# Kernel optimization log

Hardware: AMD Instinct MI355X
Metric: run time of the kernel (lower is better)

## Reference

```python
import jax, jax.numpy as jnp
import numpy as np

EPS = 1e-5

def _layernorm(x, g, b):
    mu = jnp.mean(x, axis=-1, keepdims=True)
    var = jnp.var(x, axis=-1, keepdims=True)
    return (x - mu) * jax.lax.rsqrt(var + EPS) * g + b

def setup_inputs() -> dict:
    key = jax.random.key(0)
    ks = jax.random.split(key, 12)
    E, N, H, OUT = 640000, 40000, 128, 1
    s = 1.0 / np.sqrt(H)
    s2 = 1.0 / np.sqrt(2 * H)
    return {
        "y": jax.random.normal(ks[0], (E, H), dtype=jnp.float32),
        "src": jax.random.randint(ks[1], (E,), 0, N),
        "dst": jax.random.randint(ks[2], (E,), 0, N),
        "n_nodes": N,
        "ln_g": jnp.ones((H,), jnp.float32),
        "ln_b": jnp.zeros((H,), jnp.float32),
        "Wl": jax.random.uniform(ks[3], (H, H), jnp.float32, -s, s),
        "bl": jax.random.uniform(ks[4], (H,), jnp.float32, -s, s),
        "Wr": jax.random.uniform(ks[5], (H, H), jnp.float32, -s, s),
        "br": jax.random.uniform(ks[6], (H,), jnp.float32, -s, s),
        "ln2_g": jnp.ones((2 * H,), jnp.float32),
        "ln2_b": jnp.zeros((2 * H,), jnp.float32),
        "W1": jax.random.uniform(ks[7], (2 * H, H), jnp.float32, -s2, s2),
        "b1": jax.random.uniform(ks[8], (H,), jnp.float32, -s2, s2),
        "W2": jax.random.uniform(ks[9], (H, OUT), jnp.float32, -s, s),
        "b2": jax.random.uniform(ks[10], (OUT,), jnp.float32, -s, s),
    }

def reference(y, src, dst, n_nodes, ln_g, ln_b, Wl, bl, Wr, br, ln2_g, ln2_b, W1, b1, W2, b2):
    # Gate each edge: LayerNorm -> Linear -> Sigmoid (left and right gates)
    yn = _layernorm(y, ln_g, ln_b)                       # [E, H]
    l_gate = jax.nn.sigmoid(yn @ Wl + bl)                # [E, H]
    r_gate = jax.nn.sigmoid(yn @ Wr + br)                # [E, H]
    # copy_e + mean reduce onto destination nodes (mean over incoming edges)
    cnt = jax.ops.segment_sum(jnp.ones((dst.shape[0],), y.dtype), dst, num_segments=n_nodes)
    denom = jnp.maximum(cnt, 1.0)[:, None]               # avoid div-by-zero; isolated nodes stay 0
    aleft = jax.ops.segment_sum(l_gate, dst, num_segments=n_nodes) / denom   # [N, H]
    aright = jax.ops.segment_sum(r_gate, dst, num_segments=n_nodes) / denom  # [N, H]
    # Per-edge MLP on concatenated src/dst node aggregates
    h = jnp.concatenate([aleft[src], aright[dst]], axis=1)  # [E, 2H]
    h = _layernorm(h, ln2_g, ln2_b)
    h = jax.nn.elu(h @ W1 + b1)                           # dropout is identity at inference
    return h @ W2 + b2                                    # [E, n_out]
```

## Files before the change

kernel.cpp:

```cpp
#include <hip/hip_runtime.h>
#include <hip/hip_bf16.h>

#define LN_EPS 1e-5f

typedef __attribute__((ext_vector_type(8))) short bf16x8;
typedef __attribute__((ext_vector_type(4))) float f32x4;

__device__ __forceinline__ float sigmoid_fast(float x) {
    return __builtin_amdgcn_rcpf(1.0f + __expf(-x));
}
__device__ __forceinline__ ushort f2bf(float x) {
    __hip_bfloat16 h = __float2bfloat16(x);
    return __builtin_bit_cast(ushort, h);
}
__device__ __forceinline__ int xcd_swz(int bid, int nwg) {
    const int q = nwg >> 3, r = nwg & 7;
    const int xcd = bid & 7, idx = bid >> 3;
    return (xcd < r ? xcd * (q + 1) : r * (q + 1) + (xcd - r) * q) + idx;
}
__device__ __forceinline__ int gperm(int l) {
    return (l & ~63) | (((l >> 2) & 3) << 4) | (((l >> 4) & 3) << 2) | (l & 3);
}
__device__ __forceinline__ void gload_lds16(const void* g, void* l) {
    __builtin_amdgcn_global_load_lds((const __attribute__((address_space(1))) void*)g,
                                     (__attribute__((address_space(3))) void*)l, 16, 0, 0);
}

struct WsPtrs {
    float *aggL, *aggR, *rd;
    int *ideg, *ioff, *icur, *elist, *epos;
    ushort *WgF, *W1F;
    float *gwb, *nstL, *nstR;
    int N;
};
__device__ __forceinline__ WsPtrs ws_ptrs(float* ws, const int* n_nodes_p, int E) {
    WsPtrs p;
    p.N    = *n_nodes_p;
    p.aggL = ws;
    p.aggR = ws + (size_t)p.N * 128;
    p.rd   = ws + (size_t)p.N * 256;
    p.ideg = (int*)(ws + (size_t)p.N * 257);
    p.ioff = p.ideg + p.N;
    p.icur = p.ioff + p.N + 1;
    p.elist = p.icur + p.N;
    p.epos  = p.elist + E;
    p.WgF = (ushort*)(((uintptr_t)(p.epos + E) + 15) & ~(uintptr_t)15);
    p.W1F = p.WgF + 32768;
    p.gwb = (float*)(p.W1F + 32768);
    p.nstL = p.gwb + 384;
    p.nstR = p.nstL + 2 * p.N;
    return p;
}

__global__ void init_kernel(float* __restrict__ ws, const int* __restrict__ n_nodes_p, int E) {
    WsPtrs p = ws_ptrs(ws, n_nodes_p, E);
    const long long stride = (long long)gridDim.x * blockDim.x;
    const long long tid = (long long)blockIdx.x * blockDim.x + threadIdx.x;
    const long long nf = (long long)p.N * 256;
    for (long long i = tid; i < nf; i += stride) ws[i] = 0.0f;
    for (long long i = tid; i < p.N; i += stride) p.ideg[i] = 0;
}

__global__ void hist_kernel(const int* __restrict__ dst, float* __restrict__ ws,
                            const int* __restrict__ n_nodes_p, int E) {
    WsPtrs p = ws_ptrs(ws, n_nodes_p, E);
    const int i = blockIdx.x * blockDim.x + threadIdx.x;
    if (i < E) atomicAdd(&p.ideg[dst[i]], 1);
}

__global__ __launch_bounds__(256) void scan_kernel(float* __restrict__ ws,
                                                   const int* __restrict__ n_nodes_p, int E) {
    WsPtrs p = ws_ptrs(ws, n_nodes_p, E);
    __shared__ int wsum[4];
    __shared__ int carry_s;
    const int t = threadIdx.x;
    const int lane = t & 63, wid = t >> 6;
    if (t == 0) carry_s = 0;
    __syncthreads();
    for (int base = 0; base < p.N; base += 1024) {
        const int i0 = base + t * 4;
        const int v0 = (i0 + 0 < p.N) ? p.ideg[i0 + 0] : 0;
        const int v1 = (i0 + 1 < p.N) ? p.ideg[i0 + 1] : 0;
        const int v2 = (i0 + 2 < p.N) ? p.ideg[i0 + 2] : 0;
        const int v3 = (i0 + 3 < p.N) ? p.ideg[i0 + 3] : 0;
        const int s = v0 + v1 + v2 + v3;
        int sc = s;
        #pragma unroll
        for (int off = 1; off < 64; off <<= 1) {
            const int n = __shfl_up(sc, off);
            if (lane >= off) sc += n;
        }
        if (lane == 63) wsum[wid] = sc;
        __syncthreads();
        int woff = 0;
        #pragma unroll
        for (int w = 0; w < 4; ++w) if (w < wid) woff += wsum[w];
        const int carry = carry_s;
        __syncthreads();
        const int excl = carry + woff + (sc - s);
        if (i0 + 0 < p.N) { p.ioff[i0+0] = excl;          p.icur[i0+0] = excl;          p.rd[i0+0] = 1.0f / fmaxf((float)v0, 1.0f); }
        if (i0 + 1 < p.N) { p.ioff[i0+1] = excl+v0;       p.icur[i0+1] = excl+v0;       p.rd[i0+1] = 1.0f / fmaxf((float)v1, 1.0f); }
        if (i0 + 2 < p.N) { p.ioff[i0+2] = excl+v0+v1;    p.icur[i0+2] = excl+v0+v1;    p.rd[i0+2] = 1.0f / fmaxf((float)v2, 1.0f); }
        if (i0 + 3 < p.N) { p.ioff[i0+3] = excl+v0+v1+v2; p.icur[i0+3] = excl+v0+v1+v2; p.rd[i0+3] = 1.0f / fmaxf((float)v3, 1.0f); }
        if (t == 255) carry_s = carry + woff + sc;
        __syncthreads();
    }
    if (t == 0) p.ioff[p.N] = carry_s;
}

__global__ void scatter_kernel(const int* __restrict__ dst, float* __restrict__ ws,
                               const int* __restrict__ n_nodes_p, int E) {
    WsPtrs p = ws_ptrs(ws, n_nodes_p, E);
    const int i = blockIdx.x * blockDim.x + threadIdx.x;
    if (i < E) {
        const int pos = atomicAdd(&p.icur[dst[i]], 1);
        p.elist[pos] = i;
        p.epos[i] = (pos & ~63) | gperm(pos & 63);
    }
}

__global__ void prep_w_kernel(const float* __restrict__ Wl, const float* __restrict__ Wr,
                              const float* __restrict__ W1,
                              const float* __restrict__ ln2_g, const float* __restrict__ ln2_b,
                              const float* __restrict__ b1,
                              float* __restrict__ ws, const int* __restrict__ n_nodes_p, int E) {
    WsPtrs p = ws_ptrs(ws, n_nodes_p, E);
    const int i = blockIdx.x * blockDim.x + threadIdx.x;
    if (i < 32768) {
        const int i8 = i & 7, lane = (i >> 3) & 63, kf = (i >> 9) & 3, nblk = i >> 11;
        const int k = kf * 32 + (lane >> 4) * 8 + i8;
        const int n = nblk * 16 + (lane & 15);
        const float val = (n < 128) ? Wl[k * 128 + n] : Wr[k * 128 + (n - 128)];
        p.WgF[i] = f2bf(val);
    } else if (i < 65536) {
        const int j = i - 32768;
        const int i8 = j & 7, lane = (j >> 3) & 63, kf = (j >> 9) & 7, nblk = j >> 12;
        const int k = kf * 32 + (lane >> 4) * 8 + i8;
        const int n = nblk * 16 + (lane & 15);
        p.W1F[j] = f2bf(W1[k * 128 + n]);
    } else if (i < 65664) {
        const int j = i - 65536;
        float gsL = 0.f, gsR = 0.f, bs = 0.f;
        for (int k = 0; k < 128; ++k) {
            const float wt = W1[k * 128 + j];
            const float wb = W1[(k + 128) * 128 + j];
            gsL += ln2_g[k] * wt;
            gsR += ln2_g[k + 128] * wb;
            bs  += ln2_b[k] * wt + ln2_b[k + 128] * wb;
        }
        p.gwb[j]       = gsL;
        p.gwb[128 + j] = gsR;
        p.gwb[256 + j] = bs + b1[j];
    }
}

__global__ __launch_bounds__(256) void ln_y_kernel(
    const float* __restrict__ y,
    const float* __restrict__ ln_g, const float* __restrict__ ln_b,
    float* __restrict__ ws, const int* __restrict__ n_nodes_p, int E,
    ushort* __restrict__ ynb)
{
    WsPtrs p = ws_ptrs(ws, n_nodes_p, E);
    const int t = threadIdx.x;
    const int e = blockIdx.x * 64 + (t >> 2);
    const int sub = t & 3;
    if (e >= E) return;

    const float* yr = y + (size_t)e * 128;
    float v[32];
    float s = 0.f, sq = 0.f;
    #pragma unroll
    for (int i = 0; i < 8; ++i) {
        const float4 q = *reinterpret_cast<const float4*>(yr + sub * 32 + i * 4);
        v[i*4+0] = q.x; v[i*4+1] = q.y; v[i*4+2] = q.z; v[i*4+3] = q.w;
        s  += q.x + q.y + q.z + q.w;
        sq += q.x*q.x + q.y*q.y + q.z*q.z + q.w*q.w;
    }
    s  += __shfl_xor(s, 1);  s  += __shfl_xor(s, 2);
    sq += __shfl_xor(sq, 1); sq += __shfl_xor(sq, 2);
    const float mu = s * (1.f / 128.f);
    const float rstd = rsqrtf(sq * (1.f / 128.f) - mu * mu + LN_EPS);

    ushort* dstrow = ynb + (size_t)p.epos[e] * 128 + sub * 32;
    #pragma unroll
    for (int i = 0; i < 4; ++i) {
        uint w32[4];
        #pragma unroll
        for (int h2 = 0; h2 < 4; ++h2) {
            const int c = sub * 32 + i * 8 + h2 * 2;
            const float x0 = (v[i*8 + h2*2 + 0] - mu) * rstd * ln_g[c + 0] + ln_b[c + 0];
            const float x1 = (v[i*8 + h2*2 + 1] - mu) * rstd * ln_g[c + 1] + ln_b[c + 1];
            w32[h2] = (uint)f2bf(x0) | ((uint)f2bf(x1) << 16);
        }
        *reinterpret_cast<uint4*>(dstrow + i * 8) = make_uint4(w32[0], w32[1], w32[2], w32[3]);
    }
}

__global__ __launch_bounds__(512) void gates_kernel(
    const float* __restrict__ y, const int* __restrict__ dst,
    const float* __restrict__ ln_g, const float* __restrict__ ln_b,
    const float* __restrict__ bl, const float* __restrict__ br,
    float* __restrict__ ws, const int* __restrict__ n_nodes_p, int E,
    const ushort* __restrict__ ynb)
{
    __shared__ ushort sA[128 * 128];
    __shared__ int sNode[128];

    WsPtrs p = ws_ptrs(ws, n_nodes_p, E);
    char* sAb = reinterpret_cast<char*>(sA);
    const int t = threadIdx.x;
    const int bid = xcd_swz(blockIdx.x, gridDim.x);
    const int s0 = bid * 128;
    const int lane = t & 63;
    const int w8 = t >> 6;

    if (t < 128) {
        const int j = s0 + t;
        const int eid = (j < E) ? p.elist[j] : -1;
        sNode[t] = (eid >= 0) ? dst[eid] : -1;
    }

    if (ynb) {
        const char* ybase = (const char*)ynb + (size_t)s0 * 256;
        #pragma unroll
        for (int i = 0; i < 4; ++i) {
            const int chunk = w8 + i * 8;
            const int L = chunk * 1024 + lane * 16;
            const int b = L ^ (((L >> 8) & 7) << 4);
            gload_lds16(ybase + b, sAb + chunk * 1024);
        }
    } else {
        const int r = t >> 2, sub = t & 3;
        const int je = s0 + gperm(r);
        const int eid = (je < E) ? p.elist[je] : 0;
        const float* yr = y + (size_t)eid * 128;
        float v[32];
        float s = 0.f, sq = 0.f;
        #pragma unroll
        for (int i = 0; i < 8; ++i) {
            const float4 q = *reinterpret_cast<const float4*>(yr + sub * 32 + i * 4);
            v[i*4+0] = q.x; v[i*4+1] = q.y; v[i*4+2] = q.z; v[i*4+3] = q.w;
            s  += q.x + q.y + q.z + q.w;
            sq += q.x*q.x + q.y*q.y + q.z*q.z + q.w*q.w;
        }
        s  += __shfl_xor(s, 1);  s  += __shfl_xor(s, 2);
        sq += __shfl_xor(sq, 1); sq += __shfl_xor(sq, 2);
        const float mu = s * (1.f / 128.f);
        const float rstd = rsqrtf(sq * (1.f / 128.f) - mu * mu + LN_EPS);
        #pragma unroll
        for (int i = 0; i < 4; ++i) {
            uint w32[4];
            #pragma unroll
            for (int h2 = 0; h2 < 4; ++h2) {
                const int c = sub * 32 + i * 8 + h2 * 2;
                const float x0 = (v[i*8 + h2*2 + 0] - mu) * rstd * ln_g[c + 0] + ln_b[c + 0];
                const float x1 = (v[i*8 + h2*2 + 1] - mu) * rstd * ln_g[c + 1] + ln_b[c + 1];
                w32[h2] = (uint)f2bf(x0) | ((uint)f2bf(x1) << 16);
            }
            int byte = r * 256 + sub * 64 + i * 16;
            byte ^= ((byte >> 8) & 7) << 4;
            *reinterpret_cast<uint4*>(sAb + byte) = make_uint4(w32[0], w32[1], w32[2], w32[3]);
        }
    }
    __syncthreads();

    const int rowh = w8 >> 2, colw = w8 & 3;
    const int lhi = lane >> 4, llo = lane & 15;

    f32x4 acc[4][4];
    #pragma unroll
    for (int m = 0; m < 4; ++m)
        #pragma unroll
        for (int n = 0; n < 4; ++n) acc[m][n] = (f32x4){0.f, 0.f, 0.f, 0.f};

    #pragma unroll
    for (int kf = 0; kf < 4; ++kf) {
        bf16x8 a[4], b[4];
        #pragma unroll
        for (int m = 0; m < 4; ++m) {
            const int row = rowh * 64 + m * 16 + llo;
            int byte = row * 256 + kf * 64 + lhi * 16;
            byte ^= ((byte >> 8) & 7) << 4;
            a[m] = *reinterpret_cast<const bf16x8*>(sAb + byte);
        }
        #pragma unroll
        for (int nf = 0; nf < 4; ++nf) {
            const int nblk = colw * 4 + nf;
            b[nf] = *reinterpret_cast<const bf16x8*>(p.WgF + ((size_t)(nblk * 4 + kf) * 64 + lane) * 8);
        }
        #pragma unroll
        for (int m = 0; m < 4; ++m)
            #pragma unroll
            for (int nf = 0; nf < 4; ++nf)
                acc[m][nf] = __builtin_amdgcn_mfma_f32_16x16x32_bf16(a[m], b[nf], acc[m][nf], 0, 0, 0);
    }

    const int g = colw >> 1;
    float* ag = g ? p.aggR : p.aggL;
    const float* bp = g ? br : bl;
    const int lcol0 = (colw & 1) * 64 + llo;
    float bias[4];
    #pragma unroll
    for (int nf = 0; nf < 4; ++nf) bias[nf] = bp[lcol0 + nf * 16];

    float run0 = 0.f, run1 = 0.f, run2 = 0.f, run3 = 0.f;
    int rnode = -1;
    #pragma unroll
    for (int m = 0; m < 4; ++m) {
        #pragma unroll
        for (int j = 0; j < 4; ++j) {
            const int el = rowh * 64 + lhi * 16 + m * 4 + j;
            const int node = sNode[el];
            const float v0 = sigmoid_fast(acc[m][0][j] + bias[0]);
            const float v1 = sigmoid_fast(acc[m][1][j] + bias[1]);
            const float v2 = sigmoid_fast(acc[m][2][j] + bias[2]);
            const float v3 = sigmoid_fast(acc[m][3][j] + bias[3]);
            if (node != rnode) {
                if (rnode >= 0) {
                    float* dest = ag + (size_t)rnode * 128 + lcol0;
                    atomicAdd(dest +  0, run0);
                    atomicAdd(dest + 16, run1);
                    atomicAdd(dest + 32, run2);
                    atomicAdd(dest + 48, run3);
                }
                rnode = node;
                run0 = v0; run1 = v1; run2 = v2; run3 = v3;
            } else {
                run0 += v0; run1 += v1; run2 += v2; run3 += v3;
            }
        }
    }
    if (rnode >= 0) {
        float* dest = ag + (size_t)rnode * 128 + lcol0;
        atomicAdd(dest +  0, run0);
        atomicAdd(dest + 16, run1);
        atomicAdd(dest + 32, run2);
        atomicAdd(dest + 48, run3);
    }
}

__global__ __launch_bounds__(512) void node_mlp_kernel(
    const float* __restrict__ ln2_g,
    float* __restrict__ ws, const int* __restrict__ n_nodes_p, int E)
{
    __shared__ ushort sA[128 * 256];

    WsPtrs p = ws_ptrs(ws, n_nodes_p, E);
    char* sAb = reinterpret_cast<char*>(sA);
    const int t = threadIdx.x;
    const int n0 = blockIdx.x * 128;

    {
        const int r = t >> 2, sub = t & 3;
        const int n = n0 + r;
        const bool vld = n < p.N;
        const int nn = vld ? n : (p.N - 1);
        const float* base = ((sub < 2) ? p.aggL : p.aggR) + (size_t)nn * 128 + (sub & 1) * 64;
        const float scale = vld ? p.rd[nn] : 0.f;
        const int cb = ((sub >> 1) << 7) + ((sub & 1) << 6);

        float s = 0.f, sq = 0.f;
        #pragma unroll
        for (int ii = 0; ii < 8; ++ii) {
            const float4 qa = *reinterpret_cast<const float4*>(base + ii * 8);
            const float4 qb = *reinterpret_cast<const float4*>(base + ii * 8 + 4);
            s  += qa.x + qa.y + qa.z + qa.w + qb.x + qb.y + qb.z + qb.w;
            sq += qa.x*qa.x + qa.y*qa.y + qa.z*qa.z + qa.w*qa.w
                + qb.x*qb.x + qb.y*qb.y + qb.z*qb.z + qb.w*qb.w;
        }
        s *= scale; sq *= scale * scale;
        s  += __shfl_xor(s, 1);
        sq += __shfl_xor(sq, 1);
        if (vld && sub == 0) { p.nstL[2*n] = s; p.nstL[2*n+1] = sq; }
        if (vld && sub == 2) { p.nstR[2*n] = s; p.nstR[2*n+1] = sq; }
        const float mu_n = s * (1.f / 128.f);

        #pragma unroll
        for (int ii = 0; ii < 8; ++ii) {
            const float4 qa = *reinterpret_cast<const float4*>(base + ii * 8);
            const float4 qb = *reinterpret_cast<const float4*>(base + ii * 8 + 4);
            const float xs[8] = { qa.x*scale - mu_n, qa.y*scale - mu_n, qa.z*scale - mu_n, qa.w*scale - mu_n,
                                  qb.x*scale - mu_n, qb.y*scale - mu_n, qb.z*scale - mu_n, qb.w*scale - mu_n };
            uint w32[4];
            #pragma unroll
            for (int h2 = 0; h2 < 4; ++h2) {
                const int c = cb + ii * 8 + h2 * 2;
                w32[h2] = (uint)f2bf(xs[h2*2+0] * ln2_g[c+0]) |
                          ((uint)f2bf(xs[h2*2+1] * ln2_g[c+1]) << 16);
            }
            int byte = r * 512 + cb * 2 + ii * 16;
            byte ^= ((byte >> 9) & 7) << 4;
            *reinterpret_cast<uint4*>(sAb + byte) = make_uint4(w32[0], w32[1], w32[2], w32[3]);
        }
    }
    __syncthreads();

    const int lane = t & 63;
    const int w8 = t >> 6;
    const int rowh = w8 >> 2, colw = w8 & 3;
    const int half = colw >> 1;
    const int lhi = lane >> 4, llo = lane & 15;

    f32x4 acc[4][4];
    #pragma unroll
    for (int m = 0; m < 4; ++m)
        #pragma unroll
        for (int n = 0; n < 4; ++n) acc[m][n] = (f32x4){0.f, 0.f, 0.f, 0.f};

    #pragma unroll
    for (int kfl = 0; kfl < 4; ++kfl) {
        bf16x8 a[4], b[4];
        #pragma unroll
        for (int m = 0; m < 4; ++m) {
            const int row = rowh * 64 + m * 16 + llo;
            int byte = row * 512 + half * 256 + kfl * 64 + lhi * 16;
            byte ^= ((byte >> 9) & 7) << 4;
            a[m] = *reinterpret_cast<const bf16x8*>(sAb + byte);
        }
        #pragma unroll
        for (int nf = 0; nf < 4; ++nf) {
            const int nblk = (colw & 1) * 4 + nf;
            const int kf = half * 4 + kfl;
            b[nf] = *reinterpret_cast<const bf16x8*>(p.W1F + ((size_t)(nblk * 8 + kf) * 64 + lane) * 8);
        }
        #pragma unroll
        for (int m = 0; m < 4; ++m)
            #pragma unroll
            for (int nf = 0; nf < 4; ++nf)
                acc[m][nf] = __builtin_amdgcn_mfma_f32_16x16x32_bf16(a[m], b[nf], acc[m][nf], 0, 0, 0);
    }

    ushort* u16 = (ushort*)(half ? p.aggR : p.aggL);
    #pragma unroll
    for (int m = 0; m < 4; ++m) {
        #pragma unroll
        for (int j = 0; j < 4; ++j) {
            const int n = n0 + rowh * 64 + m * 16 + lhi * 4 + j;
            if (n < p.N) {
                const int col = (colw & 1) * 64 + llo;
                #pragma unroll
                for (int nf = 0; nf < 4; ++nf)
                    u16[(size_t)n * 256 + col + nf * 16] = f2bf(acc[m][nf][j]);
            }
        }
    }
}

__global__ __launch_bounds__(256) void edge_out_kernel(
    const int* __restrict__ src, const int* __restrict__ dst,
    const float* __restrict__ W2, const float* __restrict__ b2,
    float* __restrict__ ws, const int* __restrict__ n_nodes_p,
    float* __restrict__ out, int E)
{
    WsPtrs p = ws_ptrs(ws, n_nodes_p, E);
    const ushort* uLb = (const ushort*)p.aggL;
    const ushort* uRb = (const ushort*)p.aggR;
    const int t = threadIdx.x;
    const int lane = t & 63;
    const int wv = blockIdx.x * 4 + (t >> 6);
    const int nw = gridDim.x * 4;
    const int span = (E + nw - 1) / nw;
    const int j0 = wv * span;
    const int j1 = min(E, j0 + span);

    const float2 gwl = *reinterpret_cast<const float2*>(p.gwb + lane * 2);
    const float2 gwr = *reinterpret_cast<const float2*>(p.gwb + 128 + lane * 2);
    const float2 bw  = *reinterpret_cast<const float2*>(p.gwb + 256 + lane * 2);
    const float2 w2  = *reinterpret_cast<const float2*>(W2 + lane * 2);
    const float b2v = b2[0];

    auto body = [&](int j, float& accv, int& eidv) {
        const int eid = p.elist[j];
        const int s = src[eid], d = dst[eid];
        const uint ulp = *reinterpret_cast<const uint*>(uLb + (size_t)s * 256 + lane * 2);
        const uint urp = *reinterpret_cast<const uint*>(uRb + (size_t)d * 256 + lane * 2);
        const float ulx = __builtin_bit_cast(float, ulp << 16);
        const float uly = __builtin_bit_cast(float, ulp & 0xffff0000u);
        const float urx = __builtin_bit_cast(float, urp << 16);
        const float ury = __builtin_bit_cast(float, urp & 0xffff0000u);
        const float2 nsl = *reinterpret_cast<const float2*>(p.nstL + 2 * s);
        const float2 nsr = *reinterpret_cast<const float2*>(p.nstR + 2 * d);
        const float mu = (nsl.x + nsr.x) * (1.f / 256.f);
        const float var = (nsl.y + nsr.y) * (1.f / 256.f) - mu * mu;
        const float rstd = rsqrtf(var + LN_EPS);
        const float dL = nsl.x * (1.f / 128.f) - mu;
        const float dR = nsr.x * (1.f / 128.f) - mu;
        float x0 = rstd * (ulx + urx + dL * gwl.x + dR * gwr.x) + bw.x;
        float x1 = rstd * (uly + ury + dL * gwl.y + dR * gwr.y) + bw.y;
        x0 = x0 > 0.f ? x0 : __expf(x0) - 1.f;
        x1 = x1 > 0.f ? x1 : __expf(x1) - 1.f;
        accv = x0 * w2.x + x1 * w2.y;
        eidv = eid;
    };

    int j = j0;
    for (; j + 1 < j1; j += 2) {
        float a0, a1; int e0, e1;
        body(j, a0, e0);
        body(j + 1, a1, e1);
        #pragma unroll
        for (int m = 32; m >= 1; m >>= 1) {
            a0 += __shfl_xor(a0, m);
            a1 += __shfl_xor(a1, m);
        }
        if (lane == 0) { out[e0] = a0 + b2v; out[e1] = a1 + b2v; }
    }
    if (j < j1) {
        float a0; int e0;
        body(j, a0, e0);
        #pragma unroll
        for (int m = 32; m >= 1; m >>= 1) a0 += __shfl_xor(a0, m);
        if (lane == 0) out[e0] = a0 + b2v;
    }
}

extern "C" void kernel_launch(void* const* d_in, const int* in_sizes, int n_in,
                              void* d_out, int out_size, void* d_ws, size_t ws_size,
                              hipStream_t stream) {
    const float* y       = (const float*)d_in[0];
    const int*   src     = (const int*)d_in[1];
    const int*   dst     = (const int*)d_in[2];
    const int*   n_nodes = (const int*)d_in[3];
    const float* ln_g    = (const float*)d_in[4];
    const float* ln_b    = (const float*)d_in[5];
    const float* Wl      = (const float*)d_in[6];
    const float* bl      = (const float*)d_in[7];
    const float* Wr      = (const float*)d_in[8];
    const float* br      = (const float*)d_in[9];
    const float* ln2_g   = (const float*)d_in[10];
    const float* ln2_b   = (const float*)d_in[11];
    const float* W1      = (const float*)d_in[12];
    const float* b1      = (const float*)d_in[13];
    const float* W2      = (const float*)d_in[14];
    const float* b2      = (const float*)d_in[15];
    float* out = (float*)d_out;
    float* ws  = (float*)d_ws;

    const int E = in_sizes[0] / 128;
    const int eb = (E + 127) / 128;
    const int N_MAX = 40000;

    const size_t need = (size_t)(E + 128) * 256;
    const bool use_pre = ws_size >= need + (96ull << 20);
    ushort* ynb = use_pre
        ? (ushort*)(((uintptr_t)ws + ws_size - need) & ~(uintptr_t)255)
        : nullptr;

    init_kernel<<<2048, 256, 0, stream>>>(ws, n_nodes, E);
    hist_kernel<<<(E + 255) / 256, 256, 0, stream>>>(dst, ws, n_nodes, E);
    scan_kernel<<<1, 256, 0, stream>>>(ws, n_nodes, E);
    scatter_kernel<<<(E + 255) / 256, 256, 0, stream>>>(dst, ws, n_nodes, E);
    prep_w_kernel<<<257, 256, 0, stream>>>(Wl, Wr, W1, ln2_g, ln2_b, b1, ws, n_nodes, E);
    if (use_pre)
        ln_y_kernel<<<(E + 63) / 64, 256, 0, stream>>>(y, ln_g, ln_b, ws, n_nodes, E, ynb);
    gates_kernel<<<eb, 512, 0, stream>>>(y, dst, ln_g, ln_b, bl, br, ws, n_nodes, E, ynb);
    node_mlp_kernel<<<(N_MAX + 127) / 128, 512, 0, stream>>>(ln2_g, ws, n_nodes, E);
    edge_out_kernel<<<2048, 256, 0, stream>>>(src, dst, W2, b2, ws, n_nodes, out, E);
}
```

Measured before the change: 560.0 us.

## Shrink gates tile to 64 edges per block and cache dst row in edge_out

The gates kernel now handles 64 sorted edges per 512-thread block instead of 128. Each wave covers all 64 rows and 32 output columns, which halves LDS and accumulator registers and adds a launch_bounds occupancy hint, at the cost of more blocks and reloading weight fragments per block. Separately, edge_out reuses the destination node's aggregate row and stats when consecutive edges share a dst, saving redundant gathers since edges are sorted by dst. Smaller tiles may flush more atomics at segment boundaries.

```diff
diff --git a/kernel.cpp b/kernel.cpp
--- a/kernel.cpp
+++ b/kernel.cpp
@@ -196,25 +196,25 @@
     }
 }
 
-__global__ __launch_bounds__(512) void gates_kernel(
+__global__ __launch_bounds__(512, 8) void gates_kernel(
     const float* __restrict__ y, const int* __restrict__ dst,
     const float* __restrict__ ln_g, const float* __restrict__ ln_b,
     const float* __restrict__ bl, const float* __restrict__ br,
     float* __restrict__ ws, const int* __restrict__ n_nodes_p, int E,
     const ushort* __restrict__ ynb)
 {
-    __shared__ ushort sA[128 * 128];
-    __shared__ int sNode[128];
+    __shared__ ushort sA[64 * 128];
+    __shared__ int sNode[64];
 
     WsPtrs p = ws_ptrs(ws, n_nodes_p, E);
     char* sAb = reinterpret_cast<char*>(sA);
     const int t = threadIdx.x;
     const int bid = xcd_swz(blockIdx.x, gridDim.x);
-    const int s0 = bid * 128;
+    const int s0 = bid * 64;
     const int lane = t & 63;
     const int w8 = t >> 6;
 
-    if (t < 128) {
+    if (t < 64) {
         const int j = s0 + t;
         const int eid = (j < E) ? p.elist[j] : -1;
         sNode[t] = (eid >= 0) ? dst[eid] : -1;
@@ -223,110 +223,101 @@
     if (ynb) {
         const char* ybase = (const char*)ynb + (size_t)s0 * 256;
         #pragma unroll
-        for (int i = 0; i < 4; ++i) {
-            const int chunk = w8 + i * 8;
+        for (int i = 0; i < 2; ++i) {
+            const int chunk = w8 * 2 + i;
             const int L = chunk * 1024 + lane * 16;
             const int b = L ^ (((L >> 8) & 7) << 4);
             gload_lds16(ybase + b, sAb + chunk * 1024);
         }
     } else {
-        const int r = t >> 2, sub = t & 3;
+        const int r = t >> 3, sub8 = t & 7;
         const int je = s0 + gperm(r);
         const int eid = (je < E) ? p.elist[je] : 0;
         const float* yr = y + (size_t)eid * 128;
-        float v[32];
+        float v[16];
         float s = 0.f, sq = 0.f;
         #pragma unroll
-        for (int i = 0; i < 8; ++i) {
-            const float4 q = *reinterpret_cast<const float4*>(yr + sub * 32 + i * 4);
+        for (int i = 0; i < 4; ++i) {
+            const float4 q = *reinterpret_cast<const float4*>(yr + sub8 * 16 + i * 4);
             v[i*4+0] = q.x; v[i*4+1] = q.y; v[i*4+2] = q.z; v[i*4+3] = q.w;
             s  += q.x + q.y + q.z + q.w;
             sq += q.x*q.x + q.y*q.y + q.z*q.z + q.w*q.w;
         }
-        s  += __shfl_xor(s, 1);  s  += __shfl_xor(s, 2);
-        sq += __shfl_xor(sq, 1); sq += __shfl_xor(sq, 2);
+        s  += __shfl_xor(s, 1);  s  += __shfl_xor(s, 2);  s  += __shfl_xor(s, 4);
+        sq += __shfl_xor(sq, 1); sq += __shfl_xor(sq, 2); sq += __shfl_xor(sq, 4);
         const float mu = s * (1.f / 128.f);
         const float rstd = rsqrtf(sq * (1.f / 128.f) - mu * mu + LN_EPS);
         #pragma unroll
-        for (int i = 0; i < 4; ++i) {
+        for (int i = 0; i < 2; ++i) {
             uint w32[4];
             #pragma unroll
             for (int h2 = 0; h2 < 4; ++h2) {
-                const int c = sub * 32 + i * 8 + h2 * 2;
+                const int c = sub8 * 16 + i * 8 + h2 * 2;
                 const float x0 = (v[i*8 + h2*2 + 0] - mu) * rstd * ln_g[c + 0] + ln_b[c + 0];
                 const float x1 = (v[i*8 + h2*2 + 1] - mu) * rstd * ln_g[c + 1] + ln_b[c + 1];
                 w32[h2] = (uint)f2bf(x0) | ((uint)f2bf(x1) << 16);
             }
-            int byte = r * 256 + sub * 64 + i * 16;
+            int byte = r * 256 + sub8 * 32 + i * 16;
             byte ^= ((byte >> 8) & 7) << 4;
             *reinterpret_cast<uint4*>(sAb + byte) = make_uint4(w32[0], w32[1], w32[2], w32[3]);
         }
     }
     __syncthreads();
 
-    const int rowh = w8 >> 2, colw = w8 & 3;
     const int lhi = lane >> 4, llo = lane & 15;
 
-    f32x4 acc[4][4];
+    f32x4 acc[4][2];
     #pragma unroll
     for (int m = 0; m < 4; ++m)
         #pragma unroll
-        for (int n = 0; n < 4; ++n) acc[m][n] = (f32x4){0.f, 0.f, 0.f, 0.f};
+        for (int n = 0; n < 2; ++n) acc[m][n] = (f32x4){0.f, 0.f, 0.f, 0.f};
 
     #pragma unroll
     for (int kf = 0; kf < 4; ++kf) {
-        bf16x8 a[4], b[4];
+        bf16x8 b[2];
+        #pragma unroll
+        for (int nf = 0; nf < 2; ++nf) {
+            const int nblk = w8 * 2 + nf;
+            b[nf] = *reinterpret_cast<const bf16x8*>(p.WgF + ((size_t)(nblk * 4 + kf) * 64 + lane) * 8);
+        }
         #pragma unroll
         for (int m = 0; m < 4; ++m) {
-            const int row = rowh * 64 + m * 16 + llo;
+            const int row = m * 16 + llo;
             int byte = row * 256 + kf * 64 + lhi * 16;
             byte ^= ((byte >> 8) & 7) << 4;
-            a[m] = *reinterpret_cast<const bf16x8*>(sAb + byte);
-        }
-        #pragma unroll
-        for (int nf = 0; nf < 4; ++nf) {
-            const int nblk = colw * 4 + nf;
-            b[nf] = *reinterpret_cast<const bf16x8*>(p.WgF + ((size_t)(nblk * 4 + kf) * 64 + lane) * 8);
-        }
-        #pragma unroll
-        for (int m = 0; m < 4; ++m)
-            #pragma unroll
-            for (int nf = 0; nf < 4; ++nf)
-                acc[m][nf] = __builtin_amdgcn_mfma_f32_16x16x32_bf16(a[m], b[nf], acc[m][nf], 0, 0, 0);
-    }
-
-    const int g = colw >> 1;
+            const bf16x8 a = *reinterpret_cast<const bf16x8*>(sAb + byte);
+            acc[m][0] = __builtin_amdgcn_mfma_f32_16x16x32_bf16(a, b[0], acc[m][0], 0, 0, 0);
+            acc[m][1] = __builtin_amdgcn_mfma_f32_16x16x32_bf16(a, b[1], acc[m][1], 0, 0, 0);
+        }
+    }
+
+    const int g = w8 >> 2;
     float* ag = g ? p.aggR : p.aggL;
     const float* bp = g ? br : bl;
-    const int lcol0 = (colw & 1) * 64 + llo;
-    float bias[4];
-    #pragma unroll
-    for (int nf = 0; nf < 4; ++nf) bias[nf] = bp[lcol0 + nf * 16];
-
-    float run0 = 0.f, run1 = 0.f, run2 = 0.f, run3 = 0.f;
+    const int lcol0 = (w8 & 3) * 32 + llo;
+    const float bias0 = bp[lcol0];
+    const float bias1 = bp[lcol0 + 16];
+
+    float run0 = 0.f, run1 = 0.f;
     int rnode = -1;
     #pragma unroll
     for (int m = 0; m < 4; ++m) {
         #pragma unroll
         for (int j = 0; j < 4; ++j) {
-            const int el = rowh * 64 + lhi * 16 + m * 4 + j;
+            const int el = lhi * 16 + m * 4 + j;
             const int node = sNode[el];
-            const float v0 = sigmoid_fast(acc[m][0][j] + bias[0]);
-            const float v1 = sigmoid_fast(acc[m][1][j] + bias[1]);
-            const float v2 = sigmoid_fast(acc[m][2][j] + bias[2]);
-            const float v3 = sigmoid_fast(acc[m][3][j] + bias[3]);
+            const float v0 = sigmoid_fast(acc[m][0][j] + bias0);
+            const float v1 = sigmoid_fast(acc[m][1][j] + bias1);
             if (node != rnode) {
                 if (rnode >= 0) {
                     float* dest = ag + (size_t)rnode * 128 + lcol0;
                     atomicAdd(dest +  0, run0);
                     atomicAdd(dest + 16, run1);
-                    atomicAdd(dest + 32, run2);
-                    atomicAdd(dest + 48, run3);
                 }
                 rnode = node;
-                run0 = v0; run1 = v1; run2 = v2; run3 = v3;
+                run0 = v0; run1 = v1;
             } else {
-                run0 += v0; run1 += v1; run2 += v2; run3 += v3;
+                run0 += v0; run1 += v1;
             }
         }
     }
@@ -334,8 +325,6 @@
         float* dest = ag + (size_t)rnode * 128 + lcol0;
         atomicAdd(dest +  0, run0);
         atomicAdd(dest + 16, run1);
-        atomicAdd(dest + 32, run2);
-        atomicAdd(dest + 48, run3);
     }
 }
 
@@ -469,17 +458,24 @@
     const float2 w2  = *reinterpret_cast<const float2*>(W2 + lane * 2);
     const float b2v = b2[0];
 
-    auto body = [&](int j, float& accv, int& eidv) {
-        const int eid = p.elist[j];
-        const int s = src[eid], d = dst[eid];
+    int dc = -1;
+    float urx = 0.f, ury = 0.f;
+    float2 nsr = make_float2(0.f, 0.f);
+
+    auto load_d = [&](int d) {
+        if (d != dc) {
+            const uint urp = *reinterpret_cast<const uint*>(uRb + (size_t)d * 256 + lane * 2);
+            urx = __builtin_bit_cast(float, urp << 16);
+            ury = __builtin_bit_cast(float, urp & 0xffff0000u);
+            nsr = *reinterpret_cast<const float2*>(p.nstR + 2 * d);
+            dc = d;
+        }
+    };
+    auto finish = [&](int s, float& accv) {
         const uint ulp = *reinterpret_cast<const uint*>(uLb + (size_t)s * 256 + lane * 2);
-        const uint urp = *reinterpret_cast<const uint*>(uRb + (size_t)d * 256 + lane * 2);
         const float ulx = __builtin_bit_cast(float, ulp << 16);
         const float uly = __builtin_bit_cast(float, ulp & 0xffff0000u);
-        const float urx = __builtin_bit_cast(float, urp << 16);
-        const float ury = __builtin_bit_cast(float, urp & 0xffff0000u);
         const float2 nsl = *reinterpret_cast<const float2*>(p.nstL + 2 * s);
-        const float2 nsr = *reinterpret_cast<const float2*>(p.nstR + 2 * d);
         const float mu = (nsl.x + nsr.x) * (1.f / 256.f);
         const float var = (nsl.y + nsr.y) * (1.f / 256.f) - mu * mu;
         const float rstd = rsqrtf(var + LN_EPS);
@@ -490,14 +486,18 @@
         x0 = x0 > 0.f ? x0 : __expf(x0) - 1.f;
         x1 = x1 > 0.f ? x1 : __expf(x1) - 1.f;
         accv = x0 * w2.x + x1 * w2.y;
-        eidv = eid;
     };
 
     int j = j0;
     for (; j + 1 < j1; j += 2) {
-        float a0, a1; int e0, e1;
-        body(j, a0, e0);
-        body(j + 1, a1, e1);
+        const int e0 = p.elist[j], e1 = p.elist[j + 1];
+        const int s0_ = src[e0], s1_ = src[e1];
+        const int d0_ = dst[e0], d1_ = dst[e1];
+        float a0, a1;
+        load_d(d0_);
+        finish(s0_, a0);
+        load_d(d1_);
+        finish(s1_, a1);
         #pragma unroll
         for (int m = 32; m >= 1; m >>= 1) {
             a0 += __shfl_xor(a0, m);
@@ -506,8 +506,10 @@
         if (lane == 0) { out[e0] = a0 + b2v; out[e1] = a1 + b2v; }
     }
     if (j < j1) {
-        float a0; int e0;
-        body(j, a0, e0);
+        const int e0 = p.elist[j];
+        float a0;
+        load_d(dst[e0]);
+        finish(src[e0], a0);
         #pragma unroll
         for (int m = 32; m >= 1; m >>= 1) a0 += __shfl_xor(a0, m);
         if (lane == 0) out[e0] = a0 + b2v;
@@ -537,7 +539,7 @@
     float* ws  = (float*)d_ws;
 
     const int E = in_sizes[0] / 128;
-    const int eb = (E + 127) / 128;
+    const int eb64 = (E + 63) / 64;
     const int N_MAX = 40000;
 
     const size_t need = (size_t)(E + 128) * 256;
@@ -553,7 +555,7 @@
     prep_w_kernel<<<257, 256, 0, stream>>>(Wl, Wr, W1, ln2_g, ln2_b, b1, ws, n_nodes, E);
     if (use_pre)
         ln_y_kernel<<<(E + 63) / 64, 256, 0, stream>>>(y, ln_g, ln_b, ws, n_nodes, E, ynb);
-    gates_kernel<<<eb, 512, 0, stream>>>(y, dst, ln_g, ln_b, bl, br, ws, n_nodes, E, ynb);
+    gates_kernel<<<eb64, 512, 0, stream>>>(y, dst, ln_g, ln_b, bl, br, ws, n_nodes, E, ynb);
     node_mlp_kernel<<<(N_MAX + 127) / 128, 512, 0, stream>>>(ln2_g, ws, n_nodes, E);
     edge_out_kernel<<<2048, 256, 0, stream>>>(src, dst, W2, b2, ws, n_nodes, out, E);
 }
```

Result: faster. 539.3 us (-3.7%).
